# Performance work log

Hardware: AMD Instinct MI355X
Metric: run time of the kernel (lower is better)

## Reference

```python
import jax, jax.numpy as jnp
import numpy as np

N = 50000      # nodes
R = 3          # relation types
E = 200000     # edges per relation
DIN, DHID, DOUT = 128, 128, 64


def _hetero_graphconv(x, src, dst, W, b):
    """Sum over relations of dgl GraphConv(norm='both') applied per relation.
    x:[N,d_in], src/dst:[R,E], W:[R,d_in,d_out], b:[R,d_out] -> [N,d_out]"""
    Rr, Ee = src.shape
    n = x.shape[0]
    off = (jnp.arange(Rr) * n)[:, None]            # per-relation segment offset
    src_f = (src + off).reshape(-1)                # [R*E]
    dst_f = (dst + off).reshape(-1)
    ones = jnp.ones((Rr * Ee,), x.dtype)
    out_deg = jax.ops.segment_sum(ones, src_f, num_segments=Rr * n).reshape(Rr, n)
    in_deg = jax.ops.segment_sum(ones, dst_f, num_segments=Rr * n).reshape(Rr, n)
    out_norm = jnp.maximum(out_deg, 1.0) ** -0.5   # dgl clamps deg to min 1
    in_norm = jnp.maximum(in_deg, 1.0) ** -0.5
    # gather src features, scaled by per-relation out-degree norm: [R,E,d_in]
    msgs = x[src] * jnp.take_along_axis(out_norm, src, axis=1)[..., None]
    agg = jax.ops.segment_sum(msgs.reshape(Rr * Ee, -1), dst_f,
                              num_segments=Rr * n).reshape(Rr, n, -1)
    agg = agg * in_norm[..., None]                 # [R,N,d_in]
    # per-relation linear then sum over relations (HeteroGraphConv 'sum')
    return jnp.einsum('rnd,rdo->no', agg, W) + b.sum(axis=0)


def setup_inputs() -> dict:
    key = jax.random.key(0)
    ks = jax.random.split(key, 7)
    x = jax.random.normal(ks[0], (N, DIN), jnp.float32)
    src = jax.random.randint(ks[1], (R, E), 0, N)
    dst = jax.random.randint(ks[2], (R, E), 0, N)
    W1 = jax.random.normal(ks[3], (R, DIN, DHID), jnp.float32) / np.sqrt(DIN).astype(np.float32)
    b1 = jax.random.normal(ks[4], (R, DHID), jnp.float32) * 0.01
    W2 = jax.random.normal(ks[5], (R, DHID, DOUT), jnp.float32) / np.sqrt(DHID).astype(np.float32)
    b2 = jax.random.normal(ks[6], (R, DOUT), jnp.float32) * 0.01
    return {"x": x, "W1": W1, "b1": b1, "W2": W2, "b2": b2, "src": src, "dst": dst}


def reference(x, W1, b1, W2, b2, src, dst):
    h = jax.nn.relu(_hetero_graphconv(x, src, dst, W1, b1))
    return _hetero_graphconv(h, src, dst, W2, b2)
```

## Files before the change

### kernel.cpp

```cpp
#include <hip/hip_runtime.h>

#define N_NODES 50000
#define N_REL   3
#define N_EDGE  200000
#define RN      (N_REL * N_NODES)
#define RE      (N_REL * N_EDGE)
#define GEMM1_BLKS 782
#define DEG_BLKS   2344
#define SCAN_BLOCKS 49

typedef short bf16x8 __attribute__((ext_vector_type(8)));
typedef float f32x4  __attribute__((ext_vector_type(4)));

__device__ __forceinline__ unsigned short f2bf(float f) {
    unsigned u = __float_as_uint(f);
    u = (u + 0x7fffu + ((u >> 16) & 1u)) >> 16;
    return (unsigned short)u;
}
__device__ __forceinline__ unsigned pack_bf2(float lo, float hi) {
    return (unsigned)f2bf(lo) | ((unsigned)f2bf(hi) << 16);
}

__device__ __forceinline__ void wtrans_one(
    const float* __restrict__ W, unsigned short* __restrict__ Wtf, int ncols, int i)
{
    int rel = i / (128 * ncols);
    int rem = i - rel * 128 * ncols;
    int k   = rem / ncols;
    int n   = rem - k * ncols;
    int f   = (rel * (ncols / 16) + (n >> 4)) * 4 + (k >> 5);
    int idx = f * 512 + ((k & 31) >> 3) * 128 + (n & 15) * 8 + (k & 7);
    Wtf[idx] = f2bf(W[i]);
}

__global__ __launch_bounds__(256) void wtrans2_kernel(
    const float* __restrict__ W1, unsigned short* __restrict__ Wt1,
    const float* __restrict__ W2, unsigned short* __restrict__ Wt2)
{
    int i = blockIdx.x * 256 + threadIdx.x;
    if (i < 3 * 128 * 128) {
        wtrans_one(W1, Wt1, 128, i);
    } else {
        int j = i - 3 * 128 * 128;
        if (j < 3 * 128 * 64) wtrans_one(W2, Wt2, 64, j);
    }
}

template <bool ABF16, int NCOLS>
__device__ __forceinline__ void gemm_body(
    const void* __restrict__ Av, const unsigned short* __restrict__ Wtf,
    unsigned short* __restrict__ Y, int nrows, int mt,
    unsigned* As, unsigned* Ws0, unsigned* Ws1)
{
    const int tid = threadIdx.x;
    const uint4* Wt4 = (const uint4*)Wtf;

    if constexpr (ABF16) {
        const uint4* Ab = (const uint4*)Av;
        #pragma unroll
        for (int p = 0; p < 4; ++p) {
            int q   = p * 256 + tid;
            int row = q >> 4, w4 = q & 15;
            int gr  = mt + row;
            uint4 v = make_uint4(0u, 0u, 0u, 0u);
            if (gr < nrows) v = Ab[(size_t)gr * 16 + w4];
            As[row * 68 + w4 * 4 + 0] = v.x;
            As[row * 68 + w4 * 4 + 1] = v.y;
            As[row * 68 + w4 * 4 + 2] = v.z;
            As[row * 68 + w4 * 4 + 3] = v.w;
        }
    } else {
        const float* A = (const float*)Av;
        #pragma unroll
        for (int p = 0; p < 16; ++p) {
            int q   = tid + p * 256;
            int row = q >> 6, wc = q & 63;
            int gr  = mt + row;
            float2 v = make_float2(0.f, 0.f);
            if (gr < nrows) v = *reinterpret_cast<const float2*>(&A[(size_t)gr * 128 + wc * 2]);
            As[row * 68 + wc] = pack_bf2(v.x, v.y);
        }
    }

    #pragma unroll
    for (int p = 0; p < 4; ++p) {
        uint4 v = Wt4[tid + p * 256];
        *reinterpret_cast<uint4*>(&Ws0[(tid + p * 256) * 4]) = v;
    }
    __syncthreads();

    const int w  = tid >> 6;
    const int l  = tid & 63;
    const int g  = l >> 4;
    const int lr = l & 15;
    const int ar = w * 16 + lr;

    bf16x8 a[4];
    #pragma unroll
    for (int kb = 0; kb < 4; ++kb)
        a[kb] = *reinterpret_cast<const bf16x8*>(&As[ar * 68 + kb * 16 + g * 4]);

    constexpr int TPR  = NCOLS / 16;
    constexpr int NGRP = 3 * NCOLS / 64;
    const int boff = (g * 16 + lr) * 4;

    unsigned* wc_buf = Ws0;
    unsigned* wn_buf = Ws1;
    #pragma unroll 1
    for (int grp = 0; grp < NGRP; ++grp) {
        uint4 st[4];
        if (grp + 1 < NGRP) {
            #pragma unroll
            for (int p = 0; p < 4; ++p)
                st[p] = Wt4[(grp + 1) * 1024 + tid + p * 256];
        }

        f32x4 acc[4];
        #pragma unroll
        for (int ct4 = 0; ct4 < 4; ++ct4) {
            acc[ct4] = (f32x4){0.f, 0.f, 0.f, 0.f};
            #pragma unroll
            for (int kb = 0; kb < 4; ++kb) {
                bf16x8 b = *reinterpret_cast<const bf16x8*>(
                    &wc_buf[(ct4 * 4 + kb) * 256 + boff]);
                acc[ct4] = __builtin_amdgcn_mfma_f32_16x16x32_bf16(a[kb], b, acc[ct4], 0, 0, 0);
            }
        }

        int gct0 = grp * 4;
        int rel  = gct0 / TPR;
        int cb   = (gct0 % TPR) * 16;
        #pragma unroll
        for (int i = 0; i < 4; ++i) {
            int grow = mt + w * 16 + g * 4 + i;
            if (grow < nrows) {
                size_t rowbase = ((size_t)rel * N_NODES + grow) * NCOLS + cb;
                #pragma unroll
                for (int ct4 = 0; ct4 < 4; ++ct4)
                    Y[rowbase + ct4 * 16 + lr] = f2bf(acc[ct4][i]);
            }
        }

        if (grp + 1 < NGRP) {
            #pragma unroll
            for (int p = 0; p < 4; ++p)
                *reinterpret_cast<uint4*>(&wn_buf[(tid + p * 256) * 4]) = st[p];
        }
        __syncthreads();
        unsigned* t = wc_buf; wc_buf = wn_buf; wn_buf = t;
    }
}

__global__ __launch_bounds__(256) void fused_gemm1_deg(
    const float* __restrict__ x, const unsigned short* __restrict__ Wt1,
    unsigned short* __restrict__ Y,
    const int* __restrict__ src, const int* __restrict__ dst,
    float* __restrict__ odeg, float* __restrict__ ideg)
{
    __shared__ unsigned As[64 * 68];
    __shared__ unsigned Ws[2][4096];

    if (blockIdx.x < GEMM1_BLKS) {
        gemm_body<false, 128>(x, Wt1, Y, N_NODES, blockIdx.x * 64, As, Ws[0], Ws[1]);
    } else {
        int i = (blockIdx.x - GEMM1_BLKS) * 256 + threadIdx.x;
        if (i < RE) {
            int r = i / N_EDGE;
            unsafeAtomicAdd(&odeg[r * N_NODES + src[i]], 1.0f);
            unsafeAtomicAdd(&ideg[r * N_NODES + dst[i]], 1.0f);
        }
    }
}

template <bool ABF16, int NCOLS>
__global__ __launch_bounds__(256) void gemm_mfma(
    const void* __restrict__ Av, const unsigned short* __restrict__ Wtf,
    unsigned short* __restrict__ Y, int nrows)
{
    __shared__ unsigned As[64 * 68];
    __shared__ unsigned Ws[2][4096];
    gemm_body<ABF16, NCOLS>(Av, Wtf, Y, nrows, blockIdx.x * 64, As, Ws[0], Ws[1]);
}

__global__ __launch_bounds__(256) void scan1_kernel(
    const float* __restrict__ ideg, int* __restrict__ off, int* __restrict__ bsums)
{
    __shared__ int tsum[256];
    int tid  = threadIdx.x;
    int base = blockIdx.x * 1024 + tid * 4;
    int c[4], s = 0;
    #pragma unroll
    for (int j = 0; j < 4; ++j) {
        int idx = base + j;
        c[j] = (idx < N_NODES)
             ? (int)(ideg[idx] + ideg[N_NODES + idx] + ideg[2 * N_NODES + idx]) : 0;
        s += c[j];
    }
    tsum[tid] = s;
    __syncthreads();
    #pragma unroll
    for (int d = 1; d < 256; d <<= 1) {
        int v   = tsum[tid];
        int add = (tid >= d) ? tsum[tid - d] : 0;
        __syncthreads();
        tsum[tid] = v + add;
        __syncthreads();
    }
    int run = tsum[tid] - s;
    #pragma unroll
    for (int j = 0; j < 4; ++j) {
        if (base + j < N_NODES) off[base + j] = run;
        run += c[j];
    }
    if (tid == 255) bsums[blockIdx.x] = tsum[255];
}

__global__ __launch_bounds__(256) void scan2_kernel(int* __restrict__ bsums, int nb)
{
    __shared__ int t[256];
    int tid = threadIdx.x;
    int v0  = (tid < nb) ? bsums[tid] : 0;
    t[tid] = v0;
    __syncthreads();
    #pragma unroll
    for (int d = 1; d < 256; d <<= 1) {
        int v   = t[tid];
        int add = (tid >= d) ? t[tid - d] : 0;
        __syncthreads();
        t[tid] = v + add;
        __syncthreads();
    }
    if (tid < nb) bsums[tid] = t[tid] - v0;
}

__global__ __launch_bounds__(256) void scan3_kernel(
    int* __restrict__ off, int* __restrict__ cursor, const int* __restrict__ bsums,
    float* __restrict__ odeg, float* __restrict__ ideg)
{
    int tid  = threadIdx.x;
    int base = blockIdx.x * 1024 + tid * 4;
    int add  = bsums[blockIdx.x];
    #pragma unroll
    for (int j = 0; j < 4; ++j) {
        if (base + j < N_NODES) {
            int v = off[base + j] + add;
            off[base + j]    = v;
            cursor[base + j] = v;
        }
    }
    if (blockIdx.x == 0 && tid == 0) off[N_NODES] = RE;

    int t = blockIdx.x * 256 + tid;
    for (int q = t; q < RN; q += SCAN_BLOCKS * 256) {
        odeg[q] = rsqrtf(fmaxf(odeg[q], 1.0f));
        ideg[q] = rsqrtf(fmaxf(ideg[q], 1.0f));
    }
}

__global__ __launch_bounds__(256) void fill_kernel(
    const int* __restrict__ src, const int* __restrict__ dst,
    const float* __restrict__ onorm, const float* __restrict__ inorm,
    int* __restrict__ cursor, int2* __restrict__ csr)
{
    int i = blockIdx.x * 256 + threadIdx.x;
    if (i >= N_EDGE) return;
    int r = blockIdx.y;
    int s = src[r * N_EDGE + i];
    int t = dst[r * N_EDGE + i];
    float wv = onorm[r * N_NODES + s] * inorm[r * N_NODES + t];
    int pos = atomicAdd(&cursor[t], 1);
    csr[pos] = make_int2(r * N_NODES + s, __float_as_int(wv));
}

__global__ __launch_bounds__(256) void agg128_kernel(
    const unsigned* __restrict__ Y, const int2* __restrict__ csr,
    const int* __restrict__ off, const float* __restrict__ b, unsigned* __restrict__ hbf)
{
    int wid  = (blockIdx.x * 256 + threadIdx.x) >> 6;
    int lane = threadIdx.x & 63;
    if (wid >= N_NODES) return;

    int e = off[wid], end = off[wid + 1];
    float a0 = 0.f, a1 = 0.f;

    for (; e + 8 <= end; e += 8) {
        int2 p[8]; unsigned y[8];
        #pragma unroll
        for (int j = 0; j < 8; ++j) p[j] = csr[e + j];
        #pragma unroll
        for (int j = 0; j < 8; ++j) y[j] = Y[(size_t)p[j].x * 64 + lane];
        #pragma unroll
        for (int j = 0; j < 8; ++j) {
            float wv = __int_as_float(p[j].y);
            a0 = fmaf(wv, __uint_as_float(y[j] << 16), a0);
            a1 = fmaf(wv, __uint_as_float(y[j] & 0xffff0000u), a1);
        }
    }
    if (e + 4 <= end) {
        int2 p[4]; unsigned y[4];
        #pragma unroll
        for (int j = 0; j < 4; ++j) p[j] = csr[e + j];
        #pragma unroll
        for (int j = 0; j < 4; ++j) y[j] = Y[(size_t)p[j].x * 64 + lane];
        #pragma unroll
        for (int j = 0; j < 4; ++j) {
            float wv = __int_as_float(p[j].y);
            a0 = fmaf(wv, __uint_as_float(y[j] << 16), a0);
            a1 = fmaf(wv, __uint_as_float(y[j] & 0xffff0000u), a1);
        }
        e += 4;
    }
    for (; e < end; ++e) {
        int2 p = csr[e];
        float wv = __int_as_float(p.y);
        unsigned y = Y[(size_t)p.x * 64 + lane];
        a0 = fmaf(wv, __uint_as_float(y << 16), a0);
        a1 = fmaf(wv, __uint_as_float(y & 0xffff0000u), a1);
    }

    int d = lane * 2;
    float o0 = a0 + b[d]     + b[128 + d]     + b[256 + d];
    float o1 = a1 + b[d + 1] + b[128 + d + 1] + b[256 + d + 1];
    hbf[(size_t)wid * 64 + lane] = pack_bf2(fmaxf(o0, 0.f), fmaxf(o1, 0.f));
}

__global__ __launch_bounds__(256) void agg64_kernel(
    const unsigned short* __restrict__ Y, const int2* __restrict__ csr,
    const int* __restrict__ off, const float* __restrict__ b, float* __restrict__ out)
{
    int wid  = (blockIdx.x * 256 + threadIdx.x) >> 6;
    int lane = threadIdx.x & 63;
    if (wid >= N_NODES) return;

    int e = off[wid], end = off[wid + 1];
    float a = 0.f;

    for (; e + 8 <= end; e += 8) {
        int2 p[8]; unsigned short y[8];
        #pragma unroll
        for (int j = 0; j < 8; ++j) p[j] = csr[e + j];
        #pragma unroll
        for (int j = 0; j < 8; ++j) y[j] = Y[(size_t)p[j].x * 64 + lane];
        #pragma unroll
        for (int j = 0; j < 8; ++j)
            a = fmaf(__int_as_float(p[j].y),
                     __uint_as_float(((unsigned)y[j]) << 16), a);
    }
    if (e + 4 <= end) {
        int2 p[4]; unsigned short y[4];
        #pragma unroll
        for (int j = 0; j < 4; ++j) p[j] = csr[e + j];
        #pragma unroll
        for (int j = 0; j < 4; ++j) y[j] = Y[(size_t)p[j].x * 64 + lane];
        #pragma unroll
        for (int j = 0; j < 4; ++j)
            a = fmaf(__int_as_float(p[j].y),
                     __uint_as_float(((unsigned)y[j]) << 16), a);
        e += 4;
    }
    for (; e < end; ++e) {
        int2 p = csr[e];
        a = fmaf(__int_as_float(p.y),
                 __uint_as_float(((unsigned)Y[(size_t)p.x * 64 + lane]) << 16), a);
    }

    float bs = b[lane] + b[64 + lane] + b[128 + lane];
    out[(size_t)wid * 64 + lane] = a + bs;
}

extern "C" void kernel_launch(void* const* d_in, const int* in_sizes, int n_in,
                              void* d_out, int out_size, void* d_ws, size_t ws_size,
                              hipStream_t stream)
{
    const float* x   = (const float*)d_in[0];
    const float* W1  = (const float*)d_in[1];
    const float* b1  = (const float*)d_in[2];
    const float* W2  = (const float*)d_in[3];
    const float* b2  = (const float*)d_in[4];
    const int*   src = (const int*)d_in[5];
    const int*   dst = (const int*)d_in[6];
    float*       out = (float*)d_out;

    char* w = (char*)d_ws;
    float* onorm  = (float*)w;                 w += (size_t)RN * 4;
    float* inorm  = (float*)w;                 w += (size_t)RN * 4;
    int*   off    = (int*)w;                   w += (size_t)(N_NODES + 1) * 4;
    int*   cursor = (int*)w;                   w += (size_t)N_NODES * 4;
    int*   bsums  = (int*)w;                   w += 1024;
    w = (char*)(((uintptr_t)w + 255) & ~(uintptr_t)255);
    int2*  csr    = (int2*)w;                  w += (size_t)RE * 8;
    unsigned* hbf = (unsigned*)w;              w += (size_t)N_NODES * 64 * 4;
    unsigned short* Ybf = (unsigned short*)w;  w += (size_t)N_REL * N_NODES * 128 * 2;
    unsigned short* Wt1 = (unsigned short*)w;  w += (size_t)N_REL * 128 * 128 * 2;
    unsigned short* Wt2 = (unsigned short*)w;

    wtrans2_kernel<<<(3 * 128 * 128 + 3 * 128 * 64 + 255) / 256, 256, 0, stream>>>(
        W1, Wt1, W2, Wt2);

    hipMemsetAsync(onorm, 0, (size_t)2 * RN * 4, stream);
    fused_gemm1_deg<<<GEMM1_BLKS + DEG_BLKS, 256, 0, stream>>>(
        x, Wt1, Ybf, src, dst, onorm, inorm);

    scan1_kernel<<<SCAN_BLOCKS, 256, 0, stream>>>(inorm, off, bsums);
    scan2_kernel<<<1, 256, 0, stream>>>(bsums, SCAN_BLOCKS);
    scan3_kernel<<<SCAN_BLOCKS, 256, 0, stream>>>(off, cursor, bsums, onorm, inorm);

    fill_kernel<<<dim3((N_EDGE + 255) / 256, N_REL), 256, 0, stream>>>(
        src, dst, onorm, inorm, cursor, csr);

    agg128_kernel<<<(N_NODES + 3) / 4, 256, 0, stream>>>((const unsigned*)Ybf, csr, off, b1, hbf);

    gemm_mfma<true, 64><<<GEMM1_BLKS, 256, 0, stream>>>(hbf, Wt2, Ybf, N_NODES);
    agg64_kernel<<<(N_NODES + 3) / 4, 256, 0, stream>>>(Ybf, csr, off, b2, out);
}
```

Baseline: 290.8 us.

## Record per-edge rank from degree atomics, drop cursor atomics and scan2 kernel

The degree-counting atomics now return the old in-degree, which is stored as a 16-bit per-edge rank. Together with per-relation row offsets computed in scan3, this gives each edge a deterministic CSR slot without a second atomic pass in fill. The separate scan2 kernel is removed: each scan3 block reduces the preceding block sums itself with a warp shuffle. The first GEMM is replaced by a lighter variant that keeps A in registers, uses a single W buffer, and interleaves GEMM and degree blocks in chunks of 32 so they overlap. In exchange it adds a rank array write and read, and the ranks depend on ushort range and on float atomics counting exactly.

```diff
diff --git a/kernel.cpp b/kernel.cpp
--- a/kernel.cpp
+++ b/kernel.cpp
@@ -8,6 +8,7 @@
 #define GEMM1_BLKS 782
 #define DEG_BLKS   2344
 #define SCAN_BLOCKS 49
+#define FUSE_CHUNKS 98
 
 typedef short bf16x8 __attribute__((ext_vector_type(8)));
 typedef float f32x4  __attribute__((ext_vector_type(4)));
@@ -151,35 +152,113 @@
     }
 }
 
+template <bool ABF16, int NCOLS>
+__global__ __launch_bounds__(256) void gemm_mfma(
+    const void* __restrict__ Av, const unsigned short* __restrict__ Wtf,
+    unsigned short* __restrict__ Y, int nrows)
+{
+    __shared__ unsigned As[64 * 68];
+    __shared__ unsigned Ws[2][4096];
+    gemm_body<ABF16, NCOLS>(Av, Wtf, Y, nrows, blockIdx.x * 64, As, Ws[0], Ws[1]);
+}
+
+__device__ __forceinline__ void gemm1_body_light(
+    const float* __restrict__ A, const unsigned short* __restrict__ Wtf,
+    unsigned short* __restrict__ Y, int mt, unsigned* Ws)
+{
+    const int tid = threadIdx.x;
+    const uint4* Wt4 = (const uint4*)Wtf;
+    const int w  = tid >> 6;
+    const int l  = tid & 63;
+    const int g  = l >> 4;
+    const int lr = l & 15;
+    const int arow = mt + w * 16 + lr;
+    const bool rowok = arow < N_NODES;
+
+    bf16x8 a[4];
+    #pragma unroll
+    for (int kb = 0; kb < 4; ++kb) {
+        float4 v0 = make_float4(0.f, 0.f, 0.f, 0.f);
+        float4 v1 = make_float4(0.f, 0.f, 0.f, 0.f);
+        if (rowok) {
+            const float* ap = &A[(size_t)arow * 128 + kb * 32 + g * 8];
+            v0 = *reinterpret_cast<const float4*>(ap);
+            v1 = *reinterpret_cast<const float4*>(ap + 4);
+        }
+        union { unsigned u[4]; bf16x8 v; } cv;
+        cv.u[0] = pack_bf2(v0.x, v0.y);
+        cv.u[1] = pack_bf2(v0.z, v0.w);
+        cv.u[2] = pack_bf2(v1.x, v1.y);
+        cv.u[3] = pack_bf2(v1.z, v1.w);
+        a[kb] = cv.v;
+    }
+
+    const int boff = (g * 16 + lr) * 4;
+
+    #pragma unroll 1
+    for (int grp = 0; grp < 6; ++grp) {
+        __syncthreads();
+        #pragma unroll
+        for (int p = 0; p < 4; ++p) {
+            uint4 v = Wt4[grp * 1024 + tid + p * 256];
+            *reinterpret_cast<uint4*>(&Ws[(tid + p * 256) * 4]) = v;
+        }
+        __syncthreads();
+
+        f32x4 acc[4];
+        #pragma unroll
+        for (int ct4 = 0; ct4 < 4; ++ct4) {
+            acc[ct4] = (f32x4){0.f, 0.f, 0.f, 0.f};
+            #pragma unroll
+            for (int kb = 0; kb < 4; ++kb) {
+                bf16x8 b = *reinterpret_cast<const bf16x8*>(
+                    &Ws[(ct4 * 4 + kb) * 256 + boff]);
+                acc[ct4] = __builtin_amdgcn_mfma_f32_16x16x32_bf16(a[kb], b, acc[ct4], 0, 0, 0);
+            }
+        }
+
+        int rel = grp >> 1;
+        int cb  = (grp & 1) * 64;
+        #pragma unroll
+        for (int i = 0; i < 4; ++i) {
+            int grow = mt + w * 16 + g * 4 + i;
+            if (grow < N_NODES) {
+                size_t rowbase = ((size_t)rel * N_NODES + grow) * 128 + cb;
+                #pragma unroll
+                for (int ct4 = 0; ct4 < 4; ++ct4)
+                    Y[rowbase + ct4 * 16 + lr] = f2bf(acc[ct4][i]);
+            }
+        }
+    }
+}
+
 __global__ __launch_bounds__(256) void fused_gemm1_deg(
     const float* __restrict__ x, const unsigned short* __restrict__ Wt1,
     unsigned short* __restrict__ Y,
     const int* __restrict__ src, const int* __restrict__ dst,
-    float* __restrict__ odeg, float* __restrict__ ideg)
-{
-    __shared__ unsigned As[64 * 68];
-    __shared__ unsigned Ws[2][4096];
-
-    if (blockIdx.x < GEMM1_BLKS) {
-        gemm_body<false, 128>(x, Wt1, Y, N_NODES, blockIdx.x * 64, As, Ws[0], Ws[1]);
+    float* __restrict__ odeg, float* __restrict__ ideg,
+    unsigned short* __restrict__ rank)
+{
+    __shared__ unsigned Ws[4096];
+
+    const int c = blockIdx.x >> 5;
+    const int o = blockIdx.x & 31;
+
+    if (o < 8) {
+        int gb = c * 8 + o;
+        if (gb >= GEMM1_BLKS) return;
+        gemm1_body_light(x, Wt1, Y, gb * 64, Ws);
     } else {
-        int i = (blockIdx.x - GEMM1_BLKS) * 256 + threadIdx.x;
+        int db = c * 24 + (o - 8);
+        int i  = db * 256 + threadIdx.x;
         if (i < RE) {
             int r = i / N_EDGE;
-            unsafeAtomicAdd(&odeg[r * N_NODES + src[i]], 1.0f);
-            unsafeAtomicAdd(&ideg[r * N_NODES + dst[i]], 1.0f);
-        }
-    }
-}
-
-template <bool ABF16, int NCOLS>
-__global__ __launch_bounds__(256) void gemm_mfma(
-    const void* __restrict__ Av, const unsigned short* __restrict__ Wtf,
-    unsigned short* __restrict__ Y, int nrows)
-{
-    __shared__ unsigned As[64 * 68];
-    __shared__ unsigned Ws[2][4096];
-    gemm_body<ABF16, NCOLS>(Av, Wtf, Y, nrows, blockIdx.x * 64, As, Ws[0], Ws[1]);
+            int s = src[i], t = dst[i];
+            unsafeAtomicAdd(&odeg[r * N_NODES + s], 1.0f);
+            float old = unsafeAtomicAdd(&ideg[r * N_NODES + t], 1.0f);
+            rank[i] = (unsigned short)(int)old;
+        }
+    }
 }
 
 __global__ __launch_bounds__(256) void scan1_kernel(
@@ -215,61 +294,60 @@
     if (tid == 255) bsums[blockIdx.x] = tsum[255];
 }
 
-__global__ __launch_bounds__(256) void scan2_kernel(int* __restrict__ bsums, int nb)
-{
-    __shared__ int t[256];
+__global__ __launch_bounds__(256) void scan3_kernel(
+    int* __restrict__ off, const int* __restrict__ bsums, int* __restrict__ roff,
+    float* __restrict__ odeg, float* __restrict__ ideg)
+{
+    __shared__ int addsh;
     int tid = threadIdx.x;
-    int v0  = (tid < nb) ? bsums[tid] : 0;
-    t[tid] = v0;
+    if (tid < 64) {
+        int v = (tid < blockIdx.x) ? bsums[tid] : 0;
+        #pragma unroll
+        for (int d = 32; d > 0; d >>= 1) v += __shfl_down(v, d, 64);
+        if (tid == 0) addsh = v;
+    }
     __syncthreads();
-    #pragma unroll
-    for (int d = 1; d < 256; d <<= 1) {
-        int v   = t[tid];
-        int add = (tid >= d) ? t[tid - d] : 0;
-        __syncthreads();
-        t[tid] = v + add;
-        __syncthreads();
-    }
-    if (tid < nb) bsums[tid] = t[tid] - v0;
-}
-
-__global__ __launch_bounds__(256) void scan3_kernel(
-    int* __restrict__ off, int* __restrict__ cursor, const int* __restrict__ bsums,
-    float* __restrict__ odeg, float* __restrict__ ideg)
-{
-    int tid  = threadIdx.x;
+    int add = addsh;
+
     int base = blockIdx.x * 1024 + tid * 4;
-    int add  = bsums[blockIdx.x];
     #pragma unroll
     for (int j = 0; j < 4; ++j) {
-        if (base + j < N_NODES) {
-            int v = off[base + j] + add;
-            off[base + j]    = v;
-            cursor[base + j] = v;
+        int t = base + j;
+        if (t < N_NODES) {
+            int v = off[t] + add;
+            off[t] = v;
+            float c0 = ideg[t];
+            float c1 = ideg[N_NODES + t];
+            float c2 = ideg[2 * N_NODES + t];
+            roff[t]               = v;
+            roff[N_NODES + t]     = v + (int)c0;
+            roff[2 * N_NODES + t] = v + (int)(c0 + c1);
+            ideg[t]               = rsqrtf(fmaxf(c0, 1.0f));
+            ideg[N_NODES + t]     = rsqrtf(fmaxf(c1, 1.0f));
+            ideg[2 * N_NODES + t] = rsqrtf(fmaxf(c2, 1.0f));
         }
     }
     if (blockIdx.x == 0 && tid == 0) off[N_NODES] = RE;
 
-    int t = blockIdx.x * 256 + tid;
-    for (int q = t; q < RN; q += SCAN_BLOCKS * 256) {
+    int q0 = blockIdx.x * 256 + tid;
+    for (int q = q0; q < RN; q += SCAN_BLOCKS * 256)
         odeg[q] = rsqrtf(fmaxf(odeg[q], 1.0f));
-        ideg[q] = rsqrtf(fmaxf(ideg[q], 1.0f));
-    }
 }
 
 __global__ __launch_bounds__(256) void fill_kernel(
     const int* __restrict__ src, const int* __restrict__ dst,
     const float* __restrict__ onorm, const float* __restrict__ inorm,
-    int* __restrict__ cursor, int2* __restrict__ csr)
+    const int* __restrict__ roff, const unsigned short* __restrict__ rank,
+    int2* __restrict__ csr)
 {
     int i = blockIdx.x * 256 + threadIdx.x;
     if (i >= N_EDGE) return;
-    int r = blockIdx.y;
-    int s = src[r * N_EDGE + i];
-    int t = dst[r * N_EDGE + i];
+    int r   = blockIdx.y;
+    int idx = r * N_EDGE + i;
+    int s = src[idx], t = dst[idx];
     float wv = onorm[r * N_NODES + s] * inorm[r * N_NODES + t];
-    int pos = atomicAdd(&cursor[t], 1);
-    csr[pos] = make_int2(r * N_NODES + s, __float_as_int(wv));
+    int slot = roff[r * N_NODES + t] + (int)rank[idx];
+    csr[slot] = make_int2(r * N_NODES + s, __float_as_int(wv));
 }
 
 __global__ __launch_bounds__(256) void agg128_kernel(
@@ -385,8 +463,9 @@
     float* onorm  = (float*)w;                 w += (size_t)RN * 4;
     float* inorm  = (float*)w;                 w += (size_t)RN * 4;
     int*   off    = (int*)w;                   w += (size_t)(N_NODES + 1) * 4;
-    int*   cursor = (int*)w;                   w += (size_t)N_NODES * 4;
+    int*   roff   = (int*)w;                   w += (size_t)RN * 4;
     int*   bsums  = (int*)w;                   w += 1024;
+    unsigned short* rank = (unsigned short*)w; w += (size_t)RE * 2;
     w = (char*)(((uintptr_t)w + 255) & ~(uintptr_t)255);
     int2*  csr    = (int2*)w;                  w += (size_t)RE * 8;
     unsigned* hbf = (unsigned*)w;              w += (size_t)N_NODES * 64 * 4;
@@ -398,15 +477,14 @@
         W1, Wt1, W2, Wt2);
 
     hipMemsetAsync(onorm, 0, (size_t)2 * RN * 4, stream);
-    fused_gemm1_deg<<<GEMM1_BLKS + DEG_BLKS, 256, 0, stream>>>(
-        x, Wt1, Ybf, src, dst, onorm, inorm);
+    fused_gemm1_deg<<<FUSE_CHUNKS * 32, 256, 0, stream>>>(
+        x, Wt1, Ybf, src, dst, onorm, inorm, rank);
 
     scan1_kernel<<<SCAN_BLOCKS, 256, 0, stream>>>(inorm, off, bsums);
-    scan2_kernel<<<1, 256, 0, stream>>>(bsums, SCAN_BLOCKS);
-    scan3_kernel<<<SCAN_BLOCKS, 256, 0, stream>>>(off, cursor, bsums, onorm, inorm);
+    scan3_kernel<<<SCAN_BLOCKS, 256, 0, stream>>>(off, bsums, roff, onorm, inorm);
 
     fill_kernel<<<dim3((N_EDGE + 255) / 256, N_REL), 256, 0, stream>>>(
-        src, dst, onorm, inorm, cursor, csr);
+        src, dst, onorm, inorm, roff, rank, csr);
 
     agg128_kernel<<<(N_NODES + 3) / 4, 256, 0, stream>>>((const unsigned*)Ybf, csr, off, b1, hbf);
 
```

Result: faster. 264.4 us (-9.1%).
